# Optimization experiments

Measured on AMD Instinct MI355X. Metric: run time of the kernel, lower is better.

## Reference

```python
import jax, jax.numpy as jnp
import numpy as np

N_NODES = 10000
N_EDGES = 320000
D_FEAT = 512
N_HIDDEN = 256
N_LATENT = 64


def setup_inputs() -> dict:
    key = jax.random.key(0)
    ks = jax.random.split(key, 7)
    x = jax.random.normal(ks[0], (N_NODES, D_FEAT), dtype=jnp.float32)
    edge_src = jax.random.randint(ks[1], (N_EDGES,), 0, N_NODES, dtype=jnp.int32)
    edge_dst = jax.random.randint(ks[2], (N_EDGES,), 0, N_NODES, dtype=jnp.int32)
    # positive weights, like D^{-1/2} A D^{-1/2} entries
    edge_weight = jax.random.uniform(ks[3], (N_EDGES,), dtype=jnp.float32)
    scale1 = 1.0 / np.sqrt(D_FEAT)
    scale2 = 1.0 / np.sqrt(N_HIDDEN)
    W1 = jax.random.normal(ks[4], (D_FEAT, N_HIDDEN), dtype=jnp.float32) * scale1
    W2_mu = jax.random.normal(ks[5], (N_HIDDEN, N_LATENT), dtype=jnp.float32) * scale2
    W2_sig = jax.random.normal(ks[6], (N_HIDDEN, N_LATENT), dtype=jnp.float32) * scale2
    return {"x": x, "edge_src": edge_src, "edge_dst": edge_dst,
            "edge_weight": edge_weight, "W1": W1, "W2_mu": W2_mu, "W2_sig": W2_sig}


def reference(x, edge_src, edge_dst, edge_weight, W1, W2_mu, W2_sig):
    N = x.shape[0]

    def spmm(feat):
        # sparse adj_norm @ feat via gather + weighted segment-sum
        msg = feat[edge_src] * edge_weight[:, None]           # [E, F]
        return jax.ops.segment_sum(msg, edge_dst, num_segments=N)  # [N, F]

    # GCN layer 1: relu(adj @ (x @ W1)); dropout is identity at inference
    h = jax.nn.relu(spmm(x @ W1))                              # [N, H]
    # GCN layer 2 (mu and log-sigma heads); encoder returns exp(log_sig)
    mu = spmm(h @ W2_mu)                                       # [N, L]
    sigma = jnp.exp(spmm(h @ W2_sig))                          # [N, L]
    # InnerProductDecoder: adj = z @ z.T (normalized z_ is computed but unused
    # in the original code, so it is faithfully omitted); z = mu embedding
    adj_rec = mu @ mu.T                                        # [N, N]
    return mu, sigma, adj_rec
```

## Files before the change

### kernel.cpp

```cpp
#include <hip/hip_runtime.h>
#include <hip/hip_bf16.h>
#include <math.h>
#include <float.h>

#define N_NODES 10000
#define N_EDGES 320000
#define D_FEAT  512
#define N_HID   256
#define N_LAT   64

typedef __bf16 bf16x2 __attribute__((ext_vector_type(2)));
typedef __bf16 bf16x4 __attribute__((ext_vector_type(4)));
typedef __bf16 bf16x8 __attribute__((ext_vector_type(8)));
typedef float  f32x2  __attribute__((ext_vector_type(2)));
typedef float  f32x4  __attribute__((ext_vector_type(4)));


__global__ __launch_bounds__(256) void k_hist_split(const int* __restrict__ dst,
                                                    int* __restrict__ deg8,
                                                    const float* __restrict__ x,
                                                    const float* __restrict__ W1,
                                                    const float* __restrict__ W2mu,
                                                    const float* __restrict__ W2sig,
                                                    __bf16* __restrict__ xh,
                                                    __bf16* __restrict__ xl,
                                                    __bf16* __restrict__ w1h,
                                                    __bf16* __restrict__ w1l,
                                                    __bf16* __restrict__ w2h,
                                                    __bf16* __restrict__ w2l) {
    int b = blockIdx.x;
    if (b < 1250) {
        int i = b * 256 + threadIdx.x;
        int sh = b & 7;
        if (i < N_EDGES) atomicAdd(&deg8[sh * N_NODES + dst[i]], 1);
        return;
    }
    int bb = b - 1250;
    if (bb < 5000) {
        int i = bb * 256 + threadIdx.x;
        float4 v = ((const float4*)x)[i];
        __bf16 h0 = (__bf16)v.x, h1 = (__bf16)v.y, h2 = (__bf16)v.z, h3 = (__bf16)v.w;
        bf16x4 hv = {h0, h1, h2, h3};
        bf16x4 lv = {(__bf16)(v.x - (float)h0), (__bf16)(v.y - (float)h1),
                     (__bf16)(v.z - (float)h2), (__bf16)(v.w - (float)h3)};
        ((bf16x4*)xh)[i] = hv;
        ((bf16x4*)xl)[i] = lv;
    } else {
        int i = (bb - 5000) * 256 + threadIdx.x;
        if (i < 512 * 256) {
            int j = i >> 9, k = i & 511;
            float v = W1[k * N_HID + j];
            __bf16 hi = (__bf16)v;
            w1h[i] = hi;
            w1l[i] = (__bf16)(v - (float)hi);
        } else {
            int t = i - 512 * 256;
            int j = t >> 8, k = t & 255;
            float v = (j < 64) ? W2mu[k * N_LAT + j] : W2sig[k * N_LAT + (j - 64)];
            __bf16 hi = (__bf16)v;
            w2h[t] = hi;
            w2l[t] = (__bf16)(v - (float)hi);
        }
    }
}


__global__ __launch_bounds__(1024) void k_scan8(const int* __restrict__ deg8,
                                                int* __restrict__ rowptr,
                                                int* __restrict__ woff8) {
    __shared__ int wsum[16];
    __shared__ int carry_s;
    int tid = threadIdx.x;
    if (tid == 0) carry_s = 0;
    __syncthreads();
    int lane = tid & 63, wv = tid >> 6;
    for (int base = 0; base < N_NODES; base += 1024) {
        int i = base + tid;
        int d8[8];
        int v = 0;
        #pragma unroll
        for (int s = 0; s < 8; s++) {
            d8[s] = (i < N_NODES) ? deg8[s * N_NODES + i] : 0;
            v += d8[s];
        }
        int x = v;
        #pragma unroll
        for (int off = 1; off < 64; off <<= 1) {
            int y = __shfl_up(x, off);
            if (lane >= off) x += y;
        }
        if (lane == 63) wsum[wv] = x;
        __syncthreads();
        int add = carry_s;
        for (int k = 0; k < wv; k++) add += wsum[k];
        int incl = x + add;
        int excl = incl - v;
        if (i < N_NODES) {
            rowptr[i] = excl;
            int run = excl;
            #pragma unroll
            for (int s = 0; s < 8; s++) { woff8[s * N_NODES + i] = run; run += d8[s]; }
        }
        __syncthreads();
        if (tid == 1023) carry_s = incl;
        __syncthreads();
    }
    if (tid == 0) rowptr[N_NODES] = carry_s;
}


__global__ __launch_bounds__(256) void k_scat_gemm1(const int* __restrict__ src,
                                                    const int* __restrict__ dst,
                                                    const float* __restrict__ wgt,
                                                    int* __restrict__ woff8,
                                                    int* __restrict__ esrc,
                                                    float* __restrict__ ew,
                                                    const __bf16* __restrict__ xh,
                                                    const __bf16* __restrict__ xl,
                                                    const __bf16* __restrict__ w1h,
                                                    const __bf16* __restrict__ w1l,
                                                    float* __restrict__ xw1) {
    int b = blockIdx.x;
    if (b < 1250) {
        int i = b * 256 + threadIdx.x;
        int sh = b & 7;
        if (i < N_EDGES) {
            int d = dst[i];
            int r = atomicAdd(&woff8[sh * N_NODES + d], 1);
            esrc[r] = src[i];
            ew[r] = wgt[i];
        }
        return;
    }
    int g = b - 1250;
    int bx = g & 3, by = g >> 2;
    int tid = threadIdx.x;
    int l = tid & 63, w = tid >> 6;
    int wr = w >> 1, wc = w & 1;
    int i0 = by * 128 + wr * 64;
    int j0 = bx * 64 + wc * 32;
    int lr = l & 15, lk = (l >> 4) * 8;

    f32x4 acc[4][2];
    #pragma unroll
    for (int a = 0; a < 4; a++)
        #pragma unroll
        for (int c = 0; c < 2; c++) acc[a][c] = (f32x4)(0.0f);

    #pragma unroll 4
    for (int ks = 0; ks < 16; ks++) {
        int k0 = ks * 32 + lk;
        bf16x8 ah[4], al[4], bh[2], bl[2];
        #pragma unroll
        for (int mi = 0; mi < 4; mi++) {
            int row = i0 + mi * 16 + lr;
            if (row > N_NODES - 1) row = N_NODES - 1;
            ah[mi] = *(const bf16x8*)(xh + row * D_FEAT + k0);
            al[mi] = *(const bf16x8*)(xl + row * D_FEAT + k0);
        }
        #pragma unroll
        for (int ni = 0; ni < 2; ni++) {
            int jr = j0 + ni * 16 + lr;
            bh[ni] = *(const bf16x8*)(w1h + jr * D_FEAT + k0);
            bl[ni] = *(const bf16x8*)(w1l + jr * D_FEAT + k0);
        }
        #pragma unroll
        for (int mi = 0; mi < 4; mi++)
            #pragma unroll
            for (int ni = 0; ni < 2; ni++) {
                acc[mi][ni] = __builtin_amdgcn_mfma_f32_16x16x32_bf16(ah[mi], bh[ni], acc[mi][ni], 0, 0, 0);
                acc[mi][ni] = __builtin_amdgcn_mfma_f32_16x16x32_bf16(ah[mi], bl[ni], acc[mi][ni], 0, 0, 0);
                acc[mi][ni] = __builtin_amdgcn_mfma_f32_16x16x32_bf16(al[mi], bh[ni], acc[mi][ni], 0, 0, 0);
            }
    }
    int c16 = l & 15, r4 = l >> 4;
    #pragma unroll
    for (int mi = 0; mi < 4; mi++)
        #pragma unroll
        for (int ni = 0; ni < 2; ni++)
            #pragma unroll
            for (int r = 0; r < 4; r++) {
                int row = i0 + mi * 16 + r4 * 4 + r;
                int col = j0 + ni * 16 + c16;
                if (row < N_NODES) xw1[row * N_HID + col] = acc[mi][ni][r];
            }
}


__global__ __launch_bounds__(256) void k_spmm1w(const int* __restrict__ rowptr,
                                                const int* __restrict__ esrc,
                                                const float* __restrict__ ew,
                                                const float* __restrict__ xw1,
                                                __bf16* __restrict__ hh,
                                                __bf16* __restrict__ hl) {
    int lane = threadIdx.x & 63, w = threadIdx.x >> 6;
    int n = blockIdx.x * 4 + w;
    int s = __builtin_amdgcn_readfirstlane(rowptr[n]);
    int e = __builtin_amdgcn_readfirstlane(rowptr[n + 1]);
    const float4* X = (const float4*)xw1;
    float4 acc = make_float4(0.f, 0.f, 0.f, 0.f);
    int i = s;
    for (; i + 7 < e; i += 8) {
        int   ix[8];
        float wv[8];
        #pragma unroll
        for (int u = 0; u < 8; u++) { ix[u] = esrc[i + u]; wv[u] = ew[i + u]; }
        float4 v[8];
        #pragma unroll
        for (int u = 0; u < 8; u++) v[u] = X[ix[u] * 64 + lane];
        #pragma unroll
        for (int u = 0; u < 8; u++) {
            acc.x += wv[u] * v[u].x; acc.y += wv[u] * v[u].y;
            acc.z += wv[u] * v[u].z; acc.w += wv[u] * v[u].w;
        }
    }
    for (; i + 3 < e; i += 4) {
        int s0 = esrc[i], s1 = esrc[i + 1], s2 = esrc[i + 2], s3 = esrc[i + 3];
        float w0 = ew[i], w1 = ew[i + 1], w2 = ew[i + 2], w3 = ew[i + 3];
        float4 v0 = X[s0 * 64 + lane];
        float4 v1 = X[s1 * 64 + lane];
        float4 v2 = X[s2 * 64 + lane];
        float4 v3 = X[s3 * 64 + lane];
        acc.x += w0 * v0.x + w1 * v1.x + w2 * v2.x + w3 * v3.x;
        acc.y += w0 * v0.y + w1 * v1.y + w2 * v2.y + w3 * v3.y;
        acc.z += w0 * v0.z + w1 * v1.z + w2 * v2.z + w3 * v3.z;
        acc.w += w0 * v0.w + w1 * v1.w + w2 * v2.w + w3 * v3.w;
    }
    for (; i < e; i++) {
        int sc = esrc[i]; float wv = ew[i];
        float4 v = X[sc * 64 + lane];
        acc.x += wv * v.x; acc.y += wv * v.y; acc.z += wv * v.z; acc.w += wv * v.w;
    }
    acc.x = fmaxf(acc.x, 0.f); acc.y = fmaxf(acc.y, 0.f);
    acc.z = fmaxf(acc.z, 0.f); acc.w = fmaxf(acc.w, 0.f);
    __bf16 h0 = (__bf16)acc.x, h1 = (__bf16)acc.y, h2 = (__bf16)acc.z, h3 = (__bf16)acc.w;
    bf16x4 hv = {h0, h1, h2, h3};
    bf16x4 lv = {(__bf16)(acc.x - (float)h0), (__bf16)(acc.y - (float)h1),
                 (__bf16)(acc.z - (float)h2), (__bf16)(acc.w - (float)h3)};
    ((bf16x4*)(hh + n * N_HID))[lane] = hv;
    ((bf16x4*)(hl + n * N_HID))[lane] = lv;
}


__global__ __launch_bounds__(256) void k_gemm2m(const __bf16* __restrict__ hh,
                                                const __bf16* __restrict__ hl,
                                                const __bf16* __restrict__ w2h,
                                                const __bf16* __restrict__ w2l,
                                                float* __restrict__ pre) {
    int tid = threadIdx.x;
    int l = tid & 63, w = tid >> 6;
    int wr = w >> 1, wc = w & 1;
    int i0 = blockIdx.y * 64 + wr * 32;
    int j0 = blockIdx.x * 64 + wc * 32;
    int lr = l & 15, lk = (l >> 4) * 8;

    f32x4 acc[2][2];
    #pragma unroll
    for (int a = 0; a < 2; a++)
        #pragma unroll
        for (int c = 0; c < 2; c++) acc[a][c] = (f32x4)(0.0f);

    #pragma unroll 4
    for (int ks = 0; ks < 8; ks++) {
        int k0 = ks * 32 + lk;
        bf16x8 ah[2], al[2], bh[2], bl[2];
        #pragma unroll
        for (int mi = 0; mi < 2; mi++) {
            int row = i0 + mi * 16 + lr;
            if (row > N_NODES - 1) row = N_NODES - 1;
            ah[mi] = *(const bf16x8*)(hh + row * N_HID + k0);
            al[mi] = *(const bf16x8*)(hl + row * N_HID + k0);
        }
        #pragma unroll
        for (int ni = 0; ni < 2; ni++) {
            int jr = j0 + ni * 16 + lr;
            bh[ni] = *(const bf16x8*)(w2h + jr * N_HID + k0);
            bl[ni] = *(const bf16x8*)(w2l + jr * N_HID + k0);
        }
        #pragma unroll
        for (int mi = 0; mi < 2; mi++)
            #pragma unroll
            for (int ni = 0; ni < 2; ni++) {
                acc[mi][ni] = __builtin_amdgcn_mfma_f32_16x16x32_bf16(ah[mi], bh[ni], acc[mi][ni], 0, 0, 0);
                acc[mi][ni] = __builtin_amdgcn_mfma_f32_16x16x32_bf16(ah[mi], bl[ni], acc[mi][ni], 0, 0, 0);
                acc[mi][ni] = __builtin_amdgcn_mfma_f32_16x16x32_bf16(al[mi], bh[ni], acc[mi][ni], 0, 0, 0);
            }
    }
    int c16 = l & 15, r4 = l >> 4;
    #pragma unroll
    for (int mi = 0; mi < 2; mi++)
        #pragma unroll
        for (int ni = 0; ni < 2; ni++)
            #pragma unroll
            for (int r = 0; r < 4; r++) {
                int row = i0 + mi * 16 + r4 * 4 + r;
                int col = j0 + ni * 16 + c16;
                if (row < N_NODES) pre[row * 128 + col] = acc[mi][ni][r];
            }
}


__global__ __launch_bounds__(256) void k_spmm2w(const int* __restrict__ rowptr,
                                                const int* __restrict__ esrc,
                                                const float* __restrict__ ew,
                                                const float* __restrict__ pre,
                                                float* __restrict__ out_mu,
                                                float* __restrict__ out_sig,
                                                __bf16* __restrict__ muh,
                                                __bf16* __restrict__ mul) {
    int lane = threadIdx.x & 63, w = threadIdx.x >> 6;
    int n = blockIdx.x * 4 + w;
    int s = __builtin_amdgcn_readfirstlane(rowptr[n]);
    int e = __builtin_amdgcn_readfirstlane(rowptr[n + 1]);
    const float2* P = (const float2*)pre;
    float2 acc = make_float2(0.f, 0.f);
    int i = s;
    for (; i + 3 < e; i += 4) {
        int s0 = esrc[i], s1 = esrc[i + 1], s2 = esrc[i + 2], s3 = esrc[i + 3];
        float w0 = ew[i], w1 = ew[i + 1], w2 = ew[i + 2], w3 = ew[i + 3];
        float2 v0 = P[s0 * 64 + lane];
        float2 v1 = P[s1 * 64 + lane];
        float2 v2 = P[s2 * 64 + lane];
        float2 v3 = P[s3 * 64 + lane];
        acc.x += w0 * v0.x + w1 * v1.x + w2 * v2.x + w3 * v3.x;
        acc.y += w0 * v0.y + w1 * v1.y + w2 * v2.y + w3 * v3.y;
    }
    for (; i < e; i++) {
        int sc = esrc[i]; float wv = ew[i];
        float2 v = P[sc * 64 + lane];
        acc.x += wv * v.x; acc.y += wv * v.y;
    }
    if (lane < 32) {
        ((float2*)(out_mu + n * 64))[lane] = acc;
        __bf16 h0 = (__bf16)acc.x, h1 = (__bf16)acc.y;
        bf16x2 hv = {h0, h1};
        bf16x2 lv = {(__bf16)(acc.x - (float)h0), (__bf16)(acc.y - (float)h1)};
        ((bf16x2*)(muh + n * 64))[lane] = hv;
        ((bf16x2*)(mul + n * 64))[lane] = lv;
    } else {
        float2 sg = make_float2(fminf(expf(acc.x), 3.0e38f),
                                fminf(expf(acc.y), 3.0e38f));
        ((float2*)(out_sig + n * 64))[lane - 32] = sg;
    }
}


#define ADJ_TS 68
#define ADJ_NB 6241
#define ADJ_Q  780
#define ADJ_R  1

__global__ __launch_bounds__(256) void k_adj(const __bf16* __restrict__ muh,
                                             const __bf16* __restrict__ mul,
                                             float* __restrict__ C) {
    __shared__ float Ts[4][32 * ADJ_TS];
    int g = blockIdx.x;
    int xcd = g & 7, idx = g >> 3;
    int wg = (xcd < ADJ_R ? xcd * (ADJ_Q + 1) : ADJ_R * (ADJ_Q + 1) + (xcd - ADJ_R) * ADJ_Q) + idx;
    int ti = wg / 79, tj = wg % 79;

    int tid = threadIdx.x;
    int l = tid & 63, w = tid >> 6;
    int wr = w >> 1, wc = w & 1;
    int i0 = ti * 128 + wr * 64;
    int j0 = tj * 128 + wc * 64;
    int lr = l & 15;
    int lk = (l >> 4) * 8;

    f32x4 acc[4][4];
    #pragma unroll
    for (int a = 0; a < 4; a++)
        #pragma unroll
        for (int c = 0; c < 4; c++) acc[a][c] = (f32x4)(0.0f);

    #pragma unroll
    for (int ks = 0; ks < 2; ks++) {
        int k0 = ks * 32 + lk;
        bf16x8 ah[4], al[4], bh[4], bl[4];
        #pragma unroll
        for (int mi = 0; mi < 4; mi++) {
            int row = i0 + mi * 16 + lr;
            if (row > N_NODES - 1) row = N_NODES - 1;
            ah[mi] = *(const bf16x8*)(muh + row * 64 + k0);
            al[mi] = *(const bf16x8*)(mul + row * 64 + k0);
        }
        #pragma unroll
        for (int ni = 0; ni < 4; ni++) {
            int row = j0 + ni * 16 + lr;
            if (row > N_NODES - 1) row = N_NODES - 1;
            bh[ni] = *(const bf16x8*)(muh + row * 64 + k0);
            bl[ni] = *(const bf16x8*)(mul + row * 64 + k0);
        }
        #pragma unroll
        for (int mi = 0; mi < 4; mi++)
            #pragma unroll
            for (int ni = 0; ni < 4; ni++) {
                acc[mi][ni] = __builtin_amdgcn_mfma_f32_16x16x32_bf16(ah[mi], bh[ni], acc[mi][ni], 0, 0, 0);
                acc[mi][ni] = __builtin_amdgcn_mfma_f32_16x16x32_bf16(ah[mi], bl[ni], acc[mi][ni], 0, 0, 0);
                acc[mi][ni] = __builtin_amdgcn_mfma_f32_16x16x32_bf16(al[mi], bh[ni], acc[mi][ni], 0, 0, 0);
            }
    }

    float* T = Ts[w];
    int c16 = l & 15, r4 = l >> 4;
    #pragma unroll
    for (int half = 0; half < 2; half++) {
        __syncthreads();
        #pragma unroll
        for (int m2 = 0; m2 < 2; m2++) {
            int mi = half * 2 + m2;
            #pragma unroll
            for (int ni = 0; ni < 4; ni++)
                #pragma unroll
                for (int r = 0; r < 4; r++)
                    T[(m2 * 16 + r4 * 4 + r) * ADJ_TS + ni * 16 + c16] = acc[mi][ni][r];
        }
        __syncthreads();
        #pragma unroll
        for (int q = 0; q < 8; q++) {
            int rr = q * 4 + r4;
            int row = i0 + half * 32 + rr;
            int col = j0 + c16 * 4;
            if (row < N_NODES && col < N_NODES)
                *(float4*)&C[(size_t)row * N_NODES + col] =
                    *(const float4*)&T[rr * ADJ_TS + c16 * 4];
        }
    }
}


extern "C" void kernel_launch(void* const* d_in, const int* in_sizes, int n_in,
                              void* d_out, int out_size, void* d_ws, size_t ws_size,
                              hipStream_t stream) {
    const float* x       = (const float*)d_in[0];
    const int*   esrc_in = (const int*)d_in[1];
    const int*   edst_in = (const int*)d_in[2];
    const float* ew_in   = (const float*)d_in[3];
    const float* W1      = (const float*)d_in[4];
    const float* W2mu    = (const float*)d_in[5];
    const float* W2sig   = (const float*)d_in[6];

    char* ws = (char*)d_ws;
    __bf16* xh   = (__bf16*)(ws + 0);
    __bf16* xl   = (__bf16*)(ws + 10240000);
    float*  xw1  = (float*) (ws + 20480000);
    __bf16* hh   = (__bf16*)(ws + 0);
    __bf16* hl   = (__bf16*)(ws + 5120000);
    float*  pre  = (float*) (ws + 10240000);
    __bf16* muh  = (__bf16*)(ws + 20480000);
    __bf16* mul  = (__bf16*)(ws + 21760000);
    int*    esrc = (int*)   (ws + 30720000);
    float*  ew   = (float*) (ws + 32000000);
    __bf16* w1h  = (__bf16*)(ws + 33280000);
    __bf16* w1l  = (__bf16*)(ws + 33542144);
    __bf16* w2h  = (__bf16*)(ws + 33804288);
    __bf16* w2l  = (__bf16*)(ws + 33869824);
    int*  rowptr = (int*)   (ws + 33935360);
    int*    deg8 = (int*)   (ws + 33975376);
    int*   woff8 = (int*)   (ws + 34295376);

    float* out_mu  = (float*)d_out;
    float* out_sig = out_mu + 640000;
    float* out_adj = out_sig + 640000;

    hipMemsetAsync(deg8, 0, 8 * N_NODES * sizeof(int), stream);
    k_hist_split <<<1250 + 5640, 256, 0, stream>>>(edst_in, deg8, x, W1, W2mu, W2sig,
                                                   xh, xl, w1h, w1l, w2h, w2l);
    k_scan8      <<<1, 1024, 0, stream>>>(deg8, rowptr, woff8);
    k_scat_gemm1 <<<1250 + 316, 256, 0, stream>>>(esrc_in, edst_in, ew_in, woff8,
                                                  esrc, ew, xh, xl, w1h, w1l, xw1);
    k_spmm1w     <<<N_NODES / 4, 256, 0, stream>>>(rowptr, esrc, ew, xw1, hh, hl);
    {
        dim3 g(2, 157);
        k_gemm2m <<<g, 256, 0, stream>>>(hh, hl, w2h, w2l, pre);
    }
    k_spmm2w     <<<N_NODES / 4, 256, 0, stream>>>(rowptr, esrc, ew, pre,
                                                   out_mu, out_sig, muh, mul);
    k_adj        <<<ADJ_NB, 256, 0, stream>>>(muh, mul, out_adj);
}
```

Baseline: 656.0 us.

## Shard edge-count atomics by XCC and stash ranks to drop scatter atomics

The degree histogram now shards its atomic counters by the hardware XCC id instead of by block index. Each edge's returned rank is kept in a stash array, so the scatter pass computes its CSR slot directly from the base offset plus the stored rank, with no second round of atomics. This is meant to cut cross-XCC atomic contention and remove one full set of atomics, at the cost of an extra stash write and read. It also drops the 4-wide remainder loop in the first SpMM, so leftover edges take the scalar path.

```diff
diff --git a/kernel.cpp b/kernel.cpp
--- a/kernel.cpp
+++ b/kernel.cpp
@@ -16,23 +16,35 @@
 typedef float  f32x4  __attribute__((ext_vector_type(4)));
 
 
-__global__ __launch_bounds__(256) void k_hist_split(const int* __restrict__ dst,
-                                                    int* __restrict__ deg8,
-                                                    const float* __restrict__ x,
-                                                    const float* __restrict__ W1,
-                                                    const float* __restrict__ W2mu,
-                                                    const float* __restrict__ W2sig,
-                                                    __bf16* __restrict__ xh,
-                                                    __bf16* __restrict__ xl,
-                                                    __bf16* __restrict__ w1h,
-                                                    __bf16* __restrict__ w1l,
-                                                    __bf16* __restrict__ w2h,
-                                                    __bf16* __restrict__ w2l) {
+__device__ __forceinline__ unsigned my_xcc() {
+    unsigned x;
+    asm volatile("s_getreg_b32 %0, hwreg(HW_REG_XCC_ID)" : "=s"(x));
+    return x & 7;
+}
+
+
+__global__ __launch_bounds__(256) void k_count_split(const int* __restrict__ dst,
+                                                     int* __restrict__ cntX,
+                                                     unsigned* __restrict__ stash,
+                                                     const float* __restrict__ x,
+                                                     const float* __restrict__ W1,
+                                                     const float* __restrict__ W2mu,
+                                                     const float* __restrict__ W2sig,
+                                                     __bf16* __restrict__ xh,
+                                                     __bf16* __restrict__ xl,
+                                                     __bf16* __restrict__ w1h,
+                                                     __bf16* __restrict__ w1l,
+                                                     __bf16* __restrict__ w2h,
+                                                     __bf16* __restrict__ w2l) {
     int b = blockIdx.x;
     if (b < 1250) {
         int i = b * 256 + threadIdx.x;
-        int sh = b & 7;
-        if (i < N_EDGES) atomicAdd(&deg8[sh * N_NODES + dst[i]], 1);
+        if (i < N_EDGES) {
+            unsigned xcc = my_xcc();
+            int d = dst[i];
+            int r = atomicAdd(&cntX[xcc * N_NODES + d], 1);
+            stash[i] = (xcc << 16) | (unsigned)r;
+        }
         return;
     }
     int bb = b - 1250;
@@ -65,9 +77,9 @@
 }
 
 
-__global__ __launch_bounds__(1024) void k_scan8(const int* __restrict__ deg8,
+__global__ __launch_bounds__(1024) void k_scan8(const int* __restrict__ cntX,
                                                 int* __restrict__ rowptr,
-                                                int* __restrict__ woff8) {
+                                                int* __restrict__ baseX) {
     __shared__ int wsum[16];
     __shared__ int carry_s;
     int tid = threadIdx.x;
@@ -80,7 +92,7 @@
         int v = 0;
         #pragma unroll
         for (int s = 0; s < 8; s++) {
-            d8[s] = (i < N_NODES) ? deg8[s * N_NODES + i] : 0;
+            d8[s] = (i < N_NODES) ? cntX[s * N_NODES + i] : 0;
             v += d8[s];
         }
         int x = v;
@@ -99,7 +111,7 @@
             rowptr[i] = excl;
             int run = excl;
             #pragma unroll
-            for (int s = 0; s < 8; s++) { woff8[s * N_NODES + i] = run; run += d8[s]; }
+            for (int s = 0; s < 8; s++) { baseX[s * N_NODES + i] = run; run += d8[s]; }
         }
         __syncthreads();
         if (tid == 1023) carry_s = incl;
@@ -109,26 +121,27 @@
 }
 
 
-__global__ __launch_bounds__(256) void k_scat_gemm1(const int* __restrict__ src,
-                                                    const int* __restrict__ dst,
-                                                    const float* __restrict__ wgt,
-                                                    int* __restrict__ woff8,
-                                                    int* __restrict__ esrc,
-                                                    float* __restrict__ ew,
-                                                    const __bf16* __restrict__ xh,
-                                                    const __bf16* __restrict__ xl,
-                                                    const __bf16* __restrict__ w1h,
-                                                    const __bf16* __restrict__ w1l,
-                                                    float* __restrict__ xw1) {
+__global__ __launch_bounds__(256) void k_place_gemm1(const int* __restrict__ src,
+                                                     const int* __restrict__ dst,
+                                                     const float* __restrict__ wgt,
+                                                     const int* __restrict__ baseX,
+                                                     const unsigned* __restrict__ stash,
+                                                     int* __restrict__ esrc,
+                                                     float* __restrict__ ew,
+                                                     const __bf16* __restrict__ xh,
+                                                     const __bf16* __restrict__ xl,
+                                                     const __bf16* __restrict__ w1h,
+                                                     const __bf16* __restrict__ w1l,
+                                                     float* __restrict__ xw1) {
     int b = blockIdx.x;
     if (b < 1250) {
         int i = b * 256 + threadIdx.x;
-        int sh = b & 7;
         if (i < N_EDGES) {
             int d = dst[i];
-            int r = atomicAdd(&woff8[sh * N_NODES + d], 1);
-            esrc[r] = src[i];
-            ew[r] = wgt[i];
+            unsigned st = stash[i];
+            int slot = baseX[(st >> 16) * N_NODES + d] + (int)(st & 0xFFFFu);
+            esrc[slot] = src[i];
+            ew[slot] = wgt[i];
         }
         return;
     }
@@ -213,18 +226,6 @@
             acc.x += wv[u] * v[u].x; acc.y += wv[u] * v[u].y;
             acc.z += wv[u] * v[u].z; acc.w += wv[u] * v[u].w;
         }
-    }
-    for (; i + 3 < e; i += 4) {
-        int s0 = esrc[i], s1 = esrc[i + 1], s2 = esrc[i + 2], s3 = esrc[i + 3];
-        float w0 = ew[i], w1 = ew[i + 1], w2 = ew[i + 2], w3 = ew[i + 3];
-        float4 v0 = X[s0 * 64 + lane];
-        float4 v1 = X[s1 * 64 + lane];
-        float4 v2 = X[s2 * 64 + lane];
-        float4 v3 = X[s3 * 64 + lane];
-        acc.x += w0 * v0.x + w1 * v1.x + w2 * v2.x + w3 * v3.x;
-        acc.y += w0 * v0.y + w1 * v1.y + w2 * v2.y + w3 * v3.y;
-        acc.z += w0 * v0.z + w1 * v1.z + w2 * v2.z + w3 * v3.z;
-        acc.w += w0 * v0.w + w1 * v1.w + w2 * v2.w + w3 * v3.w;
     }
     for (; i < e; i++) {
         int sc = esrc[i]; float wv = ew[i];
@@ -456,25 +457,28 @@
     __bf16* w2h  = (__bf16*)(ws + 33804288);
     __bf16* w2l  = (__bf16*)(ws + 33869824);
     int*  rowptr = (int*)   (ws + 33935360);
-    int*    deg8 = (int*)   (ws + 33975376);
-    int*   woff8 = (int*)   (ws + 34295376);
+    int*    cntX = (int*)   (ws + 33975376);
+    int*   baseX = (int*)   (ws + 34295376);
+    unsigned* stash = (unsigned*)(ws + 34615376);
 
     float* out_mu  = (float*)d_out;
     float* out_sig = out_mu + 640000;
     float* out_adj = out_sig + 640000;
 
-    hipMemsetAsync(deg8, 0, 8 * N_NODES * sizeof(int), stream);
-    k_hist_split <<<1250 + 5640, 256, 0, stream>>>(edst_in, deg8, x, W1, W2mu, W2sig,
-                                                   xh, xl, w1h, w1l, w2h, w2l);
-    k_scan8      <<<1, 1024, 0, stream>>>(deg8, rowptr, woff8);
-    k_scat_gemm1 <<<1250 + 316, 256, 0, stream>>>(esrc_in, edst_in, ew_in, woff8,
-                                                  esrc, ew, xh, xl, w1h, w1l, xw1);
-    k_spmm1w     <<<N_NODES / 4, 256, 0, stream>>>(rowptr, esrc, ew, xw1, hh, hl);
+    hipMemsetAsync(cntX, 0, 8 * N_NODES * sizeof(int), stream);
+    k_count_split <<<1250 + 5640, 256, 0, stream>>>(edst_in, cntX, stash,
+                                                    x, W1, W2mu, W2sig,
+                                                    xh, xl, w1h, w1l, w2h, w2l);
+    k_scan8       <<<1, 1024, 0, stream>>>(cntX, rowptr, baseX);
+    k_place_gemm1 <<<1250 + 316, 256, 0, stream>>>(esrc_in, edst_in, ew_in,
+                                                   baseX, stash, esrc, ew,
+                                                   xh, xl, w1h, w1l, xw1);
+    k_spmm1w      <<<N_NODES / 4, 256, 0, stream>>>(rowptr, esrc, ew, xw1, hh, hl);
     {
         dim3 g(2, 157);
-        k_gemm2m <<<g, 256, 0, stream>>>(hh, hl, w2h, w2l, pre);
-    }
-    k_spmm2w     <<<N_NODES / 4, 256, 0, stream>>>(rowptr, esrc, ew, pre,
-                                                   out_mu, out_sig, muh, mul);
-    k_adj        <<<ADJ_NB, 256, 0, stream>>>(muh, mul, out_adj);
-}
+        k_gemm2m  <<<g, 256, 0, stream>>>(hh, hl, w2h, w2l, pre);
+    }
+    k_spmm2w      <<<N_NODES / 4, 256, 0, stream>>>(rowptr, esrc, ew, pre,
+                                                    out_mu, out_sig, muh, mul);
+    k_adj         <<<ADJ_NB, 256, 0, stream>>>(muh, mul, out_adj);
+}
```

After: 656.4 us. About the same (+0.1%).
